# Kernel tuning notes

Measured on AMD Instinct MI355X. Metric: run time of the kernel, lower is better.

## Reference

```python
import jax, jax.numpy as jnp
import numpy as np

N, E = 20000, 320000          # nodes, edges (avg in-degree ~16)
F_IN, EMB, T, OUT = 40, 40, 5, 2
F_T = EMB // T                # per-tower output width = 8
EPS_STD, EPS_GN = 1e-5, 1e-5


def _lin_init(k, fan_in, fan_out, extra=()):
    return jax.random.normal(k, (*extra, fan_in, fan_out), jnp.float32) / np.sqrt(fan_in)


def setup_inputs() -> dict:
    key = jax.random.key(0)
    ks = jax.random.split(key, 8)
    # deg histogram in init: all 20000 nodes with degree 16 -> avg_deg['log'] = log(16+1)
    return dict(
        x=jax.random.normal(ks[0], (N, F_IN), jnp.float32),
        edge_index=jax.random.randint(ks[1], (2, E), 0, N),
        W_pre=_lin_init(ks[2], 2 * F_IN, F_IN, (T,)),   # per-tower pre-MLP
        b_pre=jnp.zeros((T, F_IN), jnp.float32),
        W_post=_lin_init(ks[3], 13 * F_IN, F_T, (T,)),  # (4 agg * 3 scalers + 1 residual) * F_in
        b_post=jnp.zeros((T, F_T), jnp.float32),
        W_lin=_lin_init(ks[4], T * F_T, EMB),           # PNAConv final mixing linear
        b_lin=jnp.zeros((EMB,), jnp.float32),
        gn_weight=jnp.ones((EMB,), jnp.float32),
        gn_bias=jnp.zeros((EMB,), jnp.float32),
        gn_mean_scale=jnp.ones((EMB,), jnp.float32),
        W1=_lin_init(ks[5], EMB, EMB),                  # head hidden linear
        b1=jnp.zeros((EMB,), jnp.float32),
        W2=_lin_init(ks[6], EMB, OUT),                  # head output linear
        b2=jnp.zeros((OUT,), jnp.float32),
        avg_deg_log=jnp.float32(np.log(17.0)),
    )


def _pna_conv(x, src, dst, W_pre, b_pre, W_post, b_post, W_lin, b_lin, avg_deg_log):
    xi, xj = x[dst], x[src]                              # gather: [E, F]
    h = jnp.concatenate([xi, xj], axis=-1)               # [E, 2F]
    m = jnp.einsum('ef,tfg->etg', h, W_pre) + b_pre      # per-tower messages [E, T, F]
    cnt = jax.ops.segment_sum(jnp.ones((E,), m.dtype), dst, num_segments=N)  # in-degree [N]
    denom = jnp.maximum(cnt, 1.0)[:, None, None]
    mean = jax.ops.segment_sum(m, dst, num_segments=N) / denom
    mean2 = jax.ops.segment_sum(m * m, dst, num_segments=N) / denom
    std = jnp.sqrt(jax.nn.relu(mean2 - mean * mean) + EPS_STD)
    has = (cnt > 0)[:, None, None]
    mn = jnp.where(has, jax.ops.segment_min(m, dst, num_segments=N), 0.0)
    mx = jnp.where(has, jax.ops.segment_max(m, dst, num_segments=N), 0.0)
    agg = jnp.concatenate([mean, mn, mx, std], axis=-1)  # [N, T, 4F]
    deg = jnp.maximum(cnt, 1.0)[:, None, None]
    logd = jnp.log(deg + 1.0)
    out = jnp.concatenate(
        [agg, agg * (logd / avg_deg_log), agg * (avg_deg_log / logd)], axis=-1)  # [N, T, 12F]
    out = jnp.concatenate(
        [jnp.broadcast_to(x[:, None, :], (N, T, x.shape[-1])), out], axis=-1)    # [N, T, 13F]
    out = jnp.einsum('ntf,tfg->ntg', out, W_post) + b_post                       # [N, T, F_T]
    return out.reshape(N, T * F_T) @ W_lin + b_lin


def _graph_norm(x, w, b, mean_scale):
    mean = jnp.mean(x, axis=0, keepdims=True)
    out = x - mean_scale * mean
    var = jnp.mean(out * out, axis=0, keepdims=True)
    return w * out / jnp.sqrt(var + EPS_GN) + b


def reference(x, edge_index, W_pre, b_pre, W_post, b_post, W_lin, b_lin,
              gn_weight, gn_bias, gn_mean_scale, W1, b1, W2, b2, avg_deg_log):
    src, dst = edge_index[0], edge_index[1]
    h = _pna_conv(x, src, dst, W_pre, b_pre, W_post, b_post, W_lin, b_lin, avg_deg_log)
    h = jax.nn.relu(_graph_norm(h, gn_weight, gn_bias, gn_mean_scale))
    h = jax.nn.relu(h @ W1 + b1)   # dropout_rate=None -> no dropout
    return h @ W2 + b2
```

## Files before the change

### kernel.cpp

```cpp
#include <hip/hip_runtime.h>
#include <math.h>

#define N_NODES 20000
#define N_EDGES 320000
#define F_IN 40
#define T_TOW 5
#define EMB 40
#define NPB_PRE 16
#define NBLK_MIX 313
#define NBLK_POST 79
#define PLANE (T_TOW * N_NODES * 40)
#define ECHUNK 16
#define STRIDE 64

typedef __attribute__((ext_vector_type(8))) _Float16 half8;
typedef __attribute__((ext_vector_type(4))) _Float16 half4_t;

#define WS_STATS   0
#define WS_CURSOR  320
#define WS_SSRC    80384
#define WS_MS      5200384
#define WS_MD      13200384
#define WS_AGG     21200384
#define WS_XPOST   53200384
#define WS_POSTT   56400384
#define WS_H0T     69200384
#define WS_PART    72400384

__global__ __launch_bounds__(256) void k_pre(const float* __restrict__ x,
                                             const float* __restrict__ W_pre,
                                             const float* __restrict__ b_pre,
                                             const float* __restrict__ W_post,
                                             const float* __restrict__ b_post,
                                             _Float16* __restrict__ mS,
                                             _Float16* __restrict__ mD,
                                             float* __restrict__ xpostT,
                                             int* __restrict__ cursor) {
  const int tid = threadIdx.x;
  const int n0 = blockIdx.x * NPB_PRE;
  if (tid < NPB_PRE) cursor[n0 + tid] = (n0 + tid) * STRIDE;
  const bool statlane = tid < 200;
  const int q = tid - 200;
  const bool xplane = (q >= 0 && q < 40);
  const int tc = statlane ? tid : 199;
  const int t = tc / 40, g = tc - t * 40;
  const int t2 = xplane ? q / 8 : 0, g2 = xplane ? q - (q / 8) * 8 : 0;
  float wA[40], wB[40];
  const float* Wt = W_pre + t * 3200;
#pragma unroll
  for (int j = 0; j < 40; ++j) {
    wA[j] = statlane ? Wt[j * 40 + g] : W_post[t2 * 4160 + j * 8 + g2];
    wB[j] = statlane ? Wt[(40 + j) * 40 + g] : 0.f;
  }
  const float bias = statlane ? b_pre[t * 40 + g] : b_post[t2 * 8 + g2];
  for (int ni = 0; ni < NPB_PRE; ++ni) {
    const int n = n0 + ni;
    const float* xr = x + n * F_IN;
    float aA = bias, aB = 0.f;
#pragma unroll
    for (int j = 0; j < 40; j += 4) {
      const float4 xv = *(const float4*)(xr + j);
      aA += xv.x * wA[j] + xv.y * wA[j + 1] + xv.z * wA[j + 2] + xv.w * wA[j + 3];
      aB += xv.x * wB[j] + xv.y * wB[j + 1] + xv.z * wB[j + 2] + xv.w * wB[j + 3];
    }
    if (statlane) {
      mD[n * 200 + tc] = (_Float16)aA;
      mS[n * 200 + tc] = (_Float16)aB;
    } else if (xplane) {
      xpostT[t2 * (N_NODES * 8) + n * 8 + g2] = aA;
    }
  }
}

__global__ __launch_bounds__(256) void k_scatter(const int* __restrict__ src,
                                                 const int* __restrict__ dst,
                                                 int* __restrict__ cursor,
                                                 int* __restrict__ ssrc) {
  int i = blockIdx.x * 256 + threadIdx.x;
  if (i < N_EDGES) {
    int d = dst[i];
    int pos = atomicAdd(&cursor[d], 1);
    ssrc[pos] = src[i];
  }
}

__global__ __launch_bounds__(256) void k_edge(const _Float16* __restrict__ mS,
                                              const _Float16* __restrict__ mD,
                                              const int* __restrict__ cursor,
                                              const int* __restrict__ ssrc,
                                              _Float16* __restrict__ aggS) {
  const int lane = threadIdx.x & 63;
  const int wv = threadIdx.x >> 6;
  const int n = blockIdx.x * 4 + wv;
  const int r0 = n * STRIDE;
  const int r1 = __builtin_amdgcn_readfirstlane(cursor[n]);
  const int cnt = r1 - r0;
  const bool act = lane < 50;
  const int cq = act ? lane : 49;
  const half4_t md4 = ((const half4_t*)(mD + n * 200))[cq];

  const _Float16 HINF = (_Float16)65504.f;
  half4_t sum = {0, 0, 0, 0}, ssq = {0, 0, 0, 0};
  half4_t mn = {HINF, HINF, HINF, HINF};
  half4_t mx = {-HINF, -HINF, -HINF, -HINF};
  half4_t vl4 = {0, 0, 0, 0};

  if (cnt > 0) {
    for (int p = r0; p < r1; p += ECHUNK) {
      half4_t h[ECHUNK];
#pragma unroll
      for (int i = 0; i < ECHUNK; ++i) {
        const int qe = (p + i < r1) ? (p + i) : (r1 - 1);
        const int s = __builtin_amdgcn_readfirstlane(ssrc[qe]);
        h[i] = ((const half4_t*)(mS + s * 200))[cq];
      }
#pragma unroll
      for (int i = 0; i < ECHUNK; ++i) {
        sum += h[i];
        ssq += h[i] * h[i];
        mn = __builtin_elementwise_min(mn, h[i]);
        mx = __builtin_elementwise_max(mx, h[i]);
      }
      vl4 = h[ECHUNK - 1];
    }
  }

  const int padded = ((cnt + ECHUNK - 1) / ECHUNK) * ECHUNK;
  const float d = (float)(padded - cnt);
  const float inv = (cnt > 0) ? 1.f / (float)cnt : 0.f;
  half4_t omean, omn, omx, osd;
#pragma unroll
  for (int j = 0; j < 4; ++j) {
    float mean, mnf, mxf, sd;
    if (cnt > 0) {
      const float vl = (float)vl4[j];
      const float sf = (float)sum[j] - d * vl;
      const float qf = (float)ssq[j] - d * vl * vl;
      const float msm = sf * inv;
      const float var = qf * inv - msm * msm;
      sd = sqrtf(fmaxf(var, 0.f) + 1e-5f);
      const float mdf = (float)md4[j];
      mean = mdf + msm;
      mnf = mdf + (float)mn[j];
      mxf = mdf + (float)mx[j];
    } else {
      mean = 0.f; mnf = 0.f; mxf = 0.f; sd = sqrtf(1e-5f);
    }
    omean[j] = (_Float16)mean;
    omn[j] = (_Float16)mnf;
    omx[j] = (_Float16)mxf;
    osd[j] = (_Float16)sd;
  }
  if (act) {
    const int t = cq / 10, g = 4 * (cq - t * 10);
    _Float16* a = aggS + (t * N_NODES + n) * 40 + g;
    *(half4_t*)(a) = omean;
    *(half4_t*)(a + PLANE) = omn;
    *(half4_t*)(a + 2 * PLANE) = omx;
    *(half4_t*)(a + 3 * PLANE) = osd;
  }
}

__global__ __launch_bounds__(256) void k_post(const _Float16* __restrict__ aggS,
                                              const int* __restrict__ cursor,
                                              const float* __restrict__ W_post,
                                              const float* __restrict__ avg_dl,
                                              float* __restrict__ postT4) {
  __shared__ _Float16 sAgg[256 * 42];
  const int t = blockIdx.y;
  const int s = blockIdx.z;
  const int tid = threadIdx.x;
  const int n0 = blockIdx.x * 256;
  const _Float16* gsrc = aggS + s * PLANE + (t * N_NODES + n0) * 40;
  const int lim = (N_NODES - n0) * 40;
  for (int i = 0; i < 40; ++i) {
    const int idx = tid + i * 256;
    const _Float16 vv = (idx < lim) ? gsrc[idx] : (_Float16)0.f;
    sAgg[(idx / 40) * 42 + (idx - (idx / 40) * 40)] = vv;
  }
  __syncthreads();
  const int n = n0 + tid;
  const bool ok = n < N_NODES;
  const int nn = ok ? n : N_NODES - 1;
  const int cnt = cursor[nn] - nn * STRIDE;
  const float degf = fmaxf((float)cnt, 1.f);
  const float logd = logf(degf + 1.f);
  const float avg = avg_dl[0];
  const float s1 = logd / avg, s2 = avg / logd;
  const float* Wt = W_post + t * 4160;
  float acc[8];
#pragma unroll
  for (int g2 = 0; g2 < 8; ++g2) acc[g2] = 0.f;
  const _Float16* myrow = sAgg + tid * 42;
  for (int i = 0; i < 5; ++i) {
#pragma unroll
    for (int jj = 0; jj < 8; ++jj) {
      const int kj = s * 40 + i * 8 + jj;
      const float val = (float)myrow[i * 8 + jj];
      const float* wa = Wt + (40 + kj) * 8;
      const float* wb = Wt + (200 + kj) * 8;
      const float* wc = Wt + (360 + kj) * 8;
#pragma unroll
      for (int g2 = 0; g2 < 8; ++g2)
        acc[g2] += val * (wa[g2] + s1 * wb[g2] + s2 * wc[g2]);
    }
  }
  if (ok) {
    float* pr = postT4 + ((s * T_TOW + t) * N_NODES + n) * 8;
    float4 o0 = {acc[0], acc[1], acc[2], acc[3]};
    float4 o1 = {acc[4], acc[5], acc[6], acc[7]};
    *(float4*)(pr) = o0;
    *(float4*)(pr + 4) = o1;
  }
}

__global__ __launch_bounds__(256) void k_mix(const float* __restrict__ postT4,
                                             const float* __restrict__ xpostT,
                                             const float* __restrict__ W_lin,
                                             const float* __restrict__ b_lin,
                                             float* __restrict__ h0T,
                                             float* __restrict__ partial) {
  __shared__ float sP[64 * 41];
  const int tid = threadIdx.x;
  const int n0 = blockIdx.x * 64;
  for (int i = 0; i < 10; ++i) {
    const int idx = tid + i * 256;
    const int tt = idx >> 9;
    const int r = idx & 511;
    const int row = r >> 3, c = r & 7;
    const int nn0 = n0 + row;
    const int nn = (nn0 < N_NODES) ? nn0 : 0;
    float val = xpostT[tt * (N_NODES * 8) + nn * 8 + c];
#pragma unroll
    for (int s = 0; s < 4; ++s)
      val += postT4[((s * T_TOW + tt) * N_NODES + nn) * 8 + c];
    sP[row * 41 + tt * 8 + c] = (nn0 < N_NODES) ? val : 0.f;
  }
  __syncthreads();
  const int wv = tid >> 6, lane = tid & 63;
  const int n = n0 + lane;
  const bool ok = n < N_NODES;
  for (int c = wv; c < 5; c += 4) {
    const int c0 = c * 8;
    const float4 bb0 = *(const float4*)(b_lin + c0);
    const float4 bb1 = *(const float4*)(b_lin + c0 + 4);
    float a0 = bb0.x, a1 = bb0.y, a2 = bb0.z, a3 = bb0.w;
    float a4 = bb1.x, a5 = bb1.y, a6 = bb1.z, a7 = bb1.w;
    for (int k = 0; k < 40; ++k) {
      const float p = sP[lane * 41 + k];
      const float* w = W_lin + k * EMB + c0;
      const float4 w0 = *(const float4*)(w);
      const float4 w1 = *(const float4*)(w + 4);
      a0 = fmaf(p, w0.x, a0); a1 = fmaf(p, w0.y, a1);
      a2 = fmaf(p, w0.z, a2); a3 = fmaf(p, w0.w, a3);
      a4 = fmaf(p, w1.x, a4); a5 = fmaf(p, w1.y, a5);
      a6 = fmaf(p, w1.z, a6); a7 = fmaf(p, w1.w, a7);
    }
    if (ok) {
      h0T[(c0 + 0) * N_NODES + n] = a0;
      h0T[(c0 + 1) * N_NODES + n] = a1;
      h0T[(c0 + 2) * N_NODES + n] = a2;
      h0T[(c0 + 3) * N_NODES + n] = a3;
      h0T[(c0 + 4) * N_NODES + n] = a4;
      h0T[(c0 + 5) * N_NODES + n] = a5;
      h0T[(c0 + 6) * N_NODES + n] = a6;
      h0T[(c0 + 7) * N_NODES + n] = a7;
    } else {
      a0 = a1 = a2 = a3 = a4 = a5 = a6 = a7 = 0.f;
    }
    float s[8] = {a0, a1, a2, a3, a4, a5, a6, a7};
#pragma unroll
    for (int j = 0; j < 8; ++j) {
      float sv = s[j], qv = s[j] * s[j];
#pragma unroll
      for (int m = 32; m >= 1; m >>= 1) {
        sv += __shfl_xor(sv, m, 64);
        qv += __shfl_xor(qv, m, 64);
      }
      if (lane == 0) {
        partial[blockIdx.x * 80 + c0 + j] = sv;
        partial[blockIdx.x * 80 + 40 + c0 + j] = qv;
      }
    }
  }
}

__global__ __launch_bounds__(64) void k_stats(const float* __restrict__ partial,
                                              float* __restrict__ S1,
                                              float* __restrict__ S2) {
  const int col = blockIdx.x;
  const int lane = threadIdx.x;
  float s = 0.f;
  for (int b = lane; b < NBLK_MIX; b += 64) s += partial[b * 80 + col];
#pragma unroll
  for (int m = 32; m >= 1; m >>= 1) s += __shfl_xor(s, m, 64);
  if (lane == 0) {
    if (col < 40) S1[col] = s;
    else S2[col - 40] = s;
  }
}

__global__ __launch_bounds__(256) void k_head(const float* __restrict__ h0T,
                                              const float* __restrict__ S1,
                                              const float* __restrict__ S2,
                                              const float* __restrict__ gn_w,
                                              const float* __restrict__ gn_b,
                                              const float* __restrict__ gn_ms,
                                              const float* __restrict__ W1,
                                              const float* __restrict__ b1,
                                              const float* __restrict__ W2,
                                              const float* __restrict__ b2,
                                              float* __restrict__ out) {
  __shared__ float sV[64 * 41];
  __shared__ float sH[64 * 41];
  const int tid = threadIdx.x;
  const int n0 = blockIdx.x * 64;
  const float invN = 1.f / (float)N_NODES;
  for (int i = 0; i < 10; ++i) {
    const int idx = tid + i * 256;
    const int e = idx >> 6, r = idx & 63;
    const int nn0 = n0 + r;
    const int nn = (nn0 < N_NODES) ? nn0 : 0;
    const float M = S1[e] * invN;
    const float ms = gn_ms[e];
    const float var = S2[e] * invN - ms * (2.f - ms) * M * M;
    const float sc = gn_w[e] / sqrtf(var + 1e-5f);
    const float he = h0T[e * N_NODES + nn];
    sV[r * 41 + e] = fmaxf((he - ms * M) * sc + gn_b[e], 0.f);
  }
  __syncthreads();
  const int wv = tid >> 6, lane = tid & 63;
  const int c0 = wv * 10;
  float acc[10];
#pragma unroll
  for (int j = 0; j < 10; ++j) acc[j] = b1[c0 + j];
  for (int k = 0; k < 40; ++k) {
    const float p = sV[lane * 41 + k];
    const float* w = W1 + k * EMB + c0;
#pragma unroll
    for (int j = 0; j < 10; ++j) acc[j] = fmaf(p, w[j], acc[j]);
  }
#pragma unroll
  for (int j = 0; j < 10; ++j) sH[lane * 41 + c0 + j] = fmaxf(acc[j], 0.f);
  __syncthreads();
  if (tid < 64) {
    const int n = n0 + tid;
    if (n < N_NODES) {
      float o0 = b2[0], o1 = b2[1];
      const float* hr = sH + tid * 41;
#pragma unroll
      for (int k = 0; k < 40; ++k) {
        const float r = hr[k];
        o0 = fmaf(r, W2[k * 2], o0);
        o1 = fmaf(r, W2[k * 2 + 1], o1);
      }
      out[n * 2] = o0;
      out[n * 2 + 1] = o1;
    }
  }
}

extern "C" void kernel_launch(void* const* d_in, const int* in_sizes, int n_in,
                              void* d_out, int out_size, void* d_ws, size_t ws_size,
                              hipStream_t stream) {
  const float* x      = (const float*)d_in[0];
  const int*   ei     = (const int*)d_in[1];
  const float* W_pre  = (const float*)d_in[2];
  const float* b_pre  = (const float*)d_in[3];
  const float* W_post = (const float*)d_in[4];
  const float* b_post = (const float*)d_in[5];
  const float* W_lin  = (const float*)d_in[6];
  const float* b_lin  = (const float*)d_in[7];
  const float* gn_w   = (const float*)d_in[8];
  const float* gn_b   = (const float*)d_in[9];
  const float* gn_ms  = (const float*)d_in[10];
  const float* W1     = (const float*)d_in[11];
  const float* b1     = (const float*)d_in[12];
  const float* W2     = (const float*)d_in[13];
  const float* b2     = (const float*)d_in[14];
  const float* avg_dl = (const float*)d_in[15];
  float* out = (float*)d_out;

  char* ws = (char*)d_ws;
  float* S1   = (float*)(ws + WS_STATS);
  float* S2   = S1 + 40;
  int* cursor = (int*)(ws + WS_CURSOR);
  int* ssrc   = (int*)(ws + WS_SSRC);
  _Float16* mS   = (_Float16*)(ws + WS_MS);
  _Float16* mD   = (_Float16*)(ws + WS_MD);
  _Float16* aggS = (_Float16*)(ws + WS_AGG);
  float* xpostT  = (float*)(ws + WS_XPOST);
  float* postT4  = (float*)(ws + WS_POSTT);
  float* h0T     = (float*)(ws + WS_H0T);
  float* part    = (float*)(ws + WS_PART);
  const int* e_src = ei;
  const int* e_dst = ei + N_EDGES;

  k_pre<<<N_NODES / NPB_PRE, 256, 0, stream>>>(x, W_pre, b_pre, W_post, b_post,
                                               mS, mD, xpostT, cursor);
  k_scatter<<<(N_EDGES + 255) / 256, 256, 0, stream>>>(e_src, e_dst, cursor, ssrc);
  k_edge<<<N_NODES / 4, 256, 0, stream>>>(mS, mD, cursor, ssrc, aggS);
  k_post<<<dim3(NBLK_POST, T_TOW, 4), 256, 0, stream>>>(aggS, cursor, W_post,
                                                        avg_dl, postT4);
  k_mix<<<NBLK_MIX, 256, 0, stream>>>(postT4, xpostT, W_lin, b_lin, h0T, part);
  k_stats<<<80, 64, 0, stream>>>(part, S1, S2);
  k_head<<<NBLK_MIX, 256, 0, stream>>>(h0T, S1, S2, gn_w, gn_b, gn_ms,
                                       W1, b1, W2, b2, out);
}
```

Measured before the change: 221.2 us.

## Fuse post-aggregation projection into mixing kernel, dropping postT4 intermediate

Removes the separate k_post kernel and computes the per-tower post projection inside k_mix. Each block loads the four aggregate planes for 64 nodes into shared memory, reduces the four partial sums in shared memory, and adds them to the residual term. This avoids writing and re-reading the 12.8MB postT4 buffer and saves one launch. In exchange k_mix uses more shared memory, runs only 313 blocks for this work where k_post had 1580, and adds several syncthreads per tower.

```diff
diff --git a/kernel.cpp b/kernel.cpp
--- a/kernel.cpp
+++ b/kernel.cpp
@@ -8,7 +8,6 @@
 #define EMB 40
 #define NPB_PRE 16
 #define NBLK_MIX 313
-#define NBLK_POST 79
 #define PLANE (T_TOW * N_NODES * 40)
 #define ECHUNK 16
 #define STRIDE 64
@@ -23,9 +22,8 @@
 #define WS_MD      13200384
 #define WS_AGG     21200384
 #define WS_XPOST   53200384
-#define WS_POSTT   56400384
-#define WS_H0T     69200384
-#define WS_PART    72400384
+#define WS_H0T     56400384
+#define WS_PART    59600384
 
 __global__ __launch_bounds__(256) void k_pre(const float* __restrict__ x,
                                              const float* __restrict__ W_pre,
@@ -161,83 +159,91 @@
   }
 }
 
-__global__ __launch_bounds__(256) void k_post(const _Float16* __restrict__ aggS,
-                                              const int* __restrict__ cursor,
-                                              const float* __restrict__ W_post,
-                                              const float* __restrict__ avg_dl,
-                                              float* __restrict__ postT4) {
-  __shared__ _Float16 sAgg[256 * 42];
-  const int t = blockIdx.y;
-  const int s = blockIdx.z;
-  const int tid = threadIdx.x;
-  const int n0 = blockIdx.x * 256;
-  const _Float16* gsrc = aggS + s * PLANE + (t * N_NODES + n0) * 40;
-  const int lim = (N_NODES - n0) * 40;
-  for (int i = 0; i < 40; ++i) {
-    const int idx = tid + i * 256;
-    const _Float16 vv = (idx < lim) ? gsrc[idx] : (_Float16)0.f;
-    sAgg[(idx / 40) * 42 + (idx - (idx / 40) * 40)] = vv;
-  }
-  __syncthreads();
-  const int n = n0 + tid;
-  const bool ok = n < N_NODES;
-  const int nn = ok ? n : N_NODES - 1;
-  const int cnt = cursor[nn] - nn * STRIDE;
-  const float degf = fmaxf((float)cnt, 1.f);
-  const float logd = logf(degf + 1.f);
-  const float avg = avg_dl[0];
-  const float s1 = logd / avg, s2 = avg / logd;
-  const float* Wt = W_post + t * 4160;
-  float acc[8];
-#pragma unroll
-  for (int g2 = 0; g2 < 8; ++g2) acc[g2] = 0.f;
-  const _Float16* myrow = sAgg + tid * 42;
-  for (int i = 0; i < 5; ++i) {
-#pragma unroll
-    for (int jj = 0; jj < 8; ++jj) {
-      const int kj = s * 40 + i * 8 + jj;
-      const float val = (float)myrow[i * 8 + jj];
-      const float* wa = Wt + (40 + kj) * 8;
-      const float* wb = Wt + (200 + kj) * 8;
-      const float* wc = Wt + (360 + kj) * 8;
-#pragma unroll
-      for (int g2 = 0; g2 < 8; ++g2)
-        acc[g2] += val * (wa[g2] + s1 * wb[g2] + s2 * wc[g2]);
-    }
-  }
-  if (ok) {
-    float* pr = postT4 + ((s * T_TOW + t) * N_NODES + n) * 8;
-    float4 o0 = {acc[0], acc[1], acc[2], acc[3]};
-    float4 o1 = {acc[4], acc[5], acc[6], acc[7]};
-    *(float4*)(pr) = o0;
-    *(float4*)(pr + 4) = o1;
-  }
-}
-
-__global__ __launch_bounds__(256) void k_mix(const float* __restrict__ postT4,
+__global__ __launch_bounds__(256) void k_mix(const _Float16* __restrict__ aggS,
+                                             const int* __restrict__ cursor,
+                                             const float* __restrict__ avg_dl,
                                              const float* __restrict__ xpostT,
+                                             const float* __restrict__ W_post,
                                              const float* __restrict__ W_lin,
                                              const float* __restrict__ b_lin,
                                              float* __restrict__ h0T,
                                              float* __restrict__ partial) {
   __shared__ float sP[64 * 41];
+  __shared__ _Float16 sA4[4 * 64 * 42];
+  __shared__ float sPart[4 * 64 * 8];
+  __shared__ float sS1[64], sS2[64];
   const int tid = threadIdx.x;
   const int n0 = blockIdx.x * 64;
+  if (tid < 64) {
+    const int nn0 = n0 + tid;
+    const int nn = (nn0 < N_NODES) ? nn0 : N_NODES - 1;
+    const int cnt = cursor[nn] - nn * STRIDE;
+    const float degf = fmaxf((float)cnt, 1.f);
+    const float logd = logf(degf + 1.f);
+    const float avg = avg_dl[0];
+    sS1[tid] = logd / avg;
+    sS2[tid] = avg / logd;
+  }
   for (int i = 0; i < 10; ++i) {
     const int idx = tid + i * 256;
     const int tt = idx >> 9;
-    const int r = idx & 511;
-    const int row = r >> 3, c = r & 7;
+    const int rr = idx & 511;
+    const int row = rr >> 3, c = rr & 7;
     const int nn0 = n0 + row;
     const int nn = (nn0 < N_NODES) ? nn0 : 0;
-    float val = xpostT[tt * (N_NODES * 8) + nn * 8 + c];
-#pragma unroll
-    for (int s = 0; s < 4; ++s)
-      val += postT4[((s * T_TOW + tt) * N_NODES + nn) * 8 + c];
-    sP[row * 41 + tt * 8 + c] = (nn0 < N_NODES) ? val : 0.f;
+    sP[row * 41 + tt * 8 + c] =
+        (nn0 < N_NODES) ? xpostT[tt * (N_NODES * 8) + nn * 8 + c] : 0.f;
   }
   __syncthreads();
-  const int wv = tid >> 6, lane = tid & 63;
+  const int r = tid & 63, sgp = tid >> 6;
+  for (int t = 0; t < T_TOW; ++t) {
+    for (int i = 0; i < 40; ++i) {
+      const int idx = tid + i * 256;
+      const int s = idx / 2560;
+      const int rem = idx - s * 2560;
+      const int row = rem / 40, j = rem - row * 40;
+      const int nn0 = n0 + row;
+      _Float16 v = (_Float16)0.f;
+      if (nn0 < N_NODES) v = aggS[s * PLANE + (t * N_NODES + nn0) * 40 + j];
+      sA4[(s * 64 + row) * 42 + j] = v;
+    }
+    __syncthreads();
+    {
+      const float s1 = sS1[r], s2 = sS2[r];
+      const float* Wt = W_post + t * 4160;
+      float acc[8];
+#pragma unroll
+      for (int g2 = 0; g2 < 8; ++g2) acc[g2] = 0.f;
+      const _Float16* arow = sA4 + (sgp * 64 + r) * 42;
+      for (int j = 0; j < 40; ++j) {
+        const float val = (float)arow[j];
+        const int kj = sgp * 40 + j;
+        const float* wa = Wt + (40 + kj) * 8;
+        const float* wb = Wt + (200 + kj) * 8;
+        const float* wc = Wt + (360 + kj) * 8;
+#pragma unroll
+        for (int g2 = 0; g2 < 8; ++g2)
+          acc[g2] += val * (wa[g2] + s1 * wb[g2] + s2 * wc[g2]);
+      }
+      float* pp = sPart + (sgp * 64 + r) * 8;
+#pragma unroll
+      for (int g2 = 0; g2 < 8; ++g2) pp[g2] = acc[g2];
+    }
+    __syncthreads();
+    for (int it = 0; it < 2; ++it) {
+      const int slot = tid + it * 256;
+      const int r2 = slot >> 3, g2 = slot & 7;
+      if (n0 + r2 < N_NODES) {
+        const float v = sPart[(0 * 64 + r2) * 8 + g2]
+                      + sPart[(1 * 64 + r2) * 8 + g2]
+                      + sPart[(2 * 64 + r2) * 8 + g2]
+                      + sPart[(3 * 64 + r2) * 8 + g2];
+        sP[r2 * 41 + t * 8 + g2] += v;
+      }
+    }
+    __syncthreads();
+  }
+  const int wv = sgp, lane = r;
   const int n = n0 + lane;
   const bool ok = n < N_NODES;
   for (int c = wv; c < 5; c += 4) {
@@ -390,7 +396,6 @@
   _Float16* mD   = (_Float16*)(ws + WS_MD);
   _Float16* aggS = (_Float16*)(ws + WS_AGG);
   float* xpostT  = (float*)(ws + WS_XPOST);
-  float* postT4  = (float*)(ws + WS_POSTT);
   float* h0T     = (float*)(ws + WS_H0T);
   float* part    = (float*)(ws + WS_PART);
   const int* e_src = ei;
@@ -400,9 +405,8 @@
                                                mS, mD, xpostT, cursor);
   k_scatter<<<(N_EDGES + 255) / 256, 256, 0, stream>>>(e_src, e_dst, cursor, ssrc);
   k_edge<<<N_NODES / 4, 256, 0, stream>>>(mS, mD, cursor, ssrc, aggS);
-  k_post<<<dim3(NBLK_POST, T_TOW, 4), 256, 0, stream>>>(aggS, cursor, W_post,
-                                                        avg_dl, postT4);
-  k_mix<<<NBLK_MIX, 256, 0, stream>>>(postT4, xpostT, W_lin, b_lin, h0T, part);
+  k_mix<<<NBLK_MIX, 256, 0, stream>>>(aggS, cursor, avg_dl, xpostT, W_post,
+                                      W_lin, b_lin, h0T, part);
   k_stats<<<80, 64, 0, stream>>>(part, S1, S2);
   k_head<<<NBLK_MIX, 256, 0, stream>>>(h0T, S1, S2, gn_w, gn_b, gn_ms,
                                        W1, b1, W2, b2, out);
```

New measurement: 303.5 us. 1.37x slower.
